# Kernel optimization log

Measured on AMD Instinct MI355X. Metric: run time of the kernel, lower is better.

The kernel has to match this reference:

```python
import jax, jax.numpy as jnp
import numpy as np
from jax import lax

KH = KW = 3
K = KH * KW
STRIDE = 1
PAD = 1
DIL = 1
GN_GROUPS = 32
EPS = 1e-5


def setup_inputs() -> dict:
    key = jax.random.key(0)
    k0, k1, k2 = jax.random.split(key, 3)
    B, C, H, W = 8, 256, 64, 64
    O = 256
    x = jax.random.normal(k0, (B, C, H, W), jnp.float32)
    # offset-predicting conv (DeformConv2dPack.conv_offset); small weights keep offsets ~O(1)
    w_off = jax.random.normal(k1, (2 * K, C, KH, KW), jnp.float32) * 0.01
    b_off = jnp.zeros((2 * K,), jnp.float32)
    w_dcn = jax.random.normal(k2, (O, C, KH, KW), jnp.float32) * (1.0 / np.sqrt(C * K))
    gamma = jnp.ones((O,), jnp.float32)
    beta = jnp.zeros((O,), jnp.float32)
    return {"x": x, "w_off": w_off, "b_off": b_off, "w_dcn": w_dcn, "gamma": gamma, "beta": beta}


def _deform_conv(x, w_off, b_off, w_dcn):
    B, C, H, W = x.shape
    O = w_dcn.shape[0]
    # offsets via standard conv: [B, 2K, Ho, Wo]; channel layout (k, (dy, dx))
    offset = lax.conv_general_dilated(
        x, w_off, (STRIDE, STRIDE), [(PAD, PAD), (PAD, PAD)],
        rhs_dilation=(DIL, DIL), dimension_numbers=("NCHW", "OIHW", "NCHW"))
    offset = offset + b_off[None, :, None, None]
    Ho, Wo = offset.shape[2], offset.shape[3]
    off = offset.reshape(B, K, 2, Ho, Wo)
    ky = jnp.repeat(jnp.arange(KH), KW)  # [K]
    kx = jnp.tile(jnp.arange(KW), KH)    # [K]
    base_y = (jnp.arange(Ho) * STRIDE - PAD)[None, :, None] + (ky * DIL)[:, None, None]  # [K,Ho,1]
    base_x = (jnp.arange(Wo) * STRIDE - PAD)[None, None, :] + (kx * DIL)[:, None, None]  # [K,1,Wo]
    py = off[:, :, 0] + base_y[None].astype(off.dtype)  # [B,K,Ho,Wo]
    px = off[:, :, 1] + base_x[None].astype(off.dtype)

    def sample_one(xi, py_i, px_i):  # xi [C,H,W]; py/px [K,Ho,Wo]
        y0 = jnp.floor(py_i)
        x0 = jnp.floor(px_i)
        dy = py_i - y0
        dx = px_i - x0
        y0i = y0.astype(jnp.int32)
        x0i = x0.astype(jnp.int32)

        def gather(yi, xj, w):
            valid = (yi >= 0) & (yi < H) & (xj >= 0) & (xj < W)
            yc = jnp.clip(yi, 0, H - 1)
            xc = jnp.clip(xj, 0, W - 1)
            return xi[:, yc, xc] * (w * valid)[None]  # [C,K,Ho,Wo]

        return (gather(y0i, x0i, (1 - dy) * (1 - dx))
                + gather(y0i, x0i + 1, (1 - dy) * dx)
                + gather(y0i + 1, x0i, dy * (1 - dx))
                + gather(y0i + 1, x0i + 1, dy * dx))

    cols = jax.vmap(sample_one)(x, py, px)  # [B,C,K,Ho,Wo]
    y = jnp.einsum("ock,bckp->bop", w_dcn.reshape(O, C, K),
                   cols.reshape(B, C, K, Ho * Wo))
    return y.reshape(B, O, Ho, Wo)


def _group_norm(y, gamma, beta):
    B, O, Ho, Wo = y.shape
    g = y.reshape(B, GN_GROUPS, O // GN_GROUPS, Ho, Wo)
    mean = g.mean(axis=(2, 3, 4), keepdims=True)
    var = g.var(axis=(2, 3, 4), keepdims=True)
    yn = ((g - mean) * lax.rsqrt(var + EPS)).reshape(B, O, Ho, Wo)
    return yn * gamma[None, :, None, None] + beta[None, :, None, None]


def reference(x, w_off, b_off, w_dcn, gamma, beta):
    y = _deform_conv(x, w_off, b_off, w_dcn)
    y = _group_norm(y, gamma, beta)
    return y * jnp.tanh(jax.nn.softplus(y))  # Mish
```

## Files before the change

### kernel.cpp

```cpp
#include <hip/hip_runtime.h>
#include <hip/hip_bf16.h>
#include <math.h>

typedef __bf16 bf16x8 __attribute__((ext_vector_type(8)));
typedef float f32x4 __attribute__((ext_vector_type(4)));
typedef unsigned int u32;
typedef u32 u32x4 __attribute__((ext_vector_type(4)));
typedef u32 u32x2 __attribute__((ext_vector_type(2)));


__device__ inline u32 pack2bf16(float a, float b) {
  u32 ua = __float_as_uint(a);
  u32 ub = __float_as_uint(b);
  ua += 0x7fffu + ((ua >> 16) & 1u);
  ub += 0x7fffu + ((ub >> 16) & 1u);
  return (ua >> 16) | (ub & 0xffff0000u);
}

__global__ void prep(const float* __restrict__ w_dcn, const float* __restrict__ w_off,
                     unsigned short* __restrict__ wT4, unsigned short* __restrict__ wOffT,
                     float* __restrict__ stats) {
  size_t id = (size_t)blockIdx.x * 256 + threadIdx.x;
  if (id < 589824) {
    int o  = (int)(id / 2304);
    int ck = (int)(id % 2304);
    int k = ck >> 8, c = ck & 255;
    float v = w_dcn[(size_t)(o * 256 + c) * 9 + k];
    u32 uv = __float_as_uint(v);
    uv += 0x7fffu + ((uv >> 16) & 1u);
    int tile = ck >> 6, kk = ck & 63;
    int lin = o * 128 + kk * 2;
    int swz = lin ^ ((o & 7) << 4);
    *(unsigned short*)((char*)wT4 + (size_t)tile * 32768 + swz) = (unsigned short)(uv >> 16);
  } else if (id < 663552) {
    int r = (int)(id - 589824);
    int tile = r >> 11;
    int rr = r & 2047;
    int o = rr >> 6, kk = rr & 63;
    int k = tile >> 2, cc = tile & 3;
    int c = (cc << 6) + kk;
    float v = (o < 18) ? w_off[(size_t)(o * 256 + c) * 9 + k] : 0.f;
    u32 uv = __float_as_uint(v);
    uv += 0x7fffu + ((uv >> 16) & 1u);
    int swz = (o * 128 + kk * 2) ^ ((o & 7) << 4);
    *(unsigned short*)((char*)wOffT + (size_t)tile * 4096 + swz) = (unsigned short)(uv >> 16);
  } else if (id < 664064) {
    stats[id - 663552] = 0.f;
  }
}

__global__ __launch_bounds__(256) void transpose_x(const float* __restrict__ x,
                                                   unsigned short* __restrict__ xT) {
  __shared__ float tl[64][65];
  int bx = blockIdx.x;
  int b = bx >> 8;
  int y = (bx >> 2) & 63;
  int cb = (bx & 3) << 6;
  int t = threadIdx.x;
  int xi = t & 63, cr = t >> 6;
  size_t base = (((size_t)(b * 256 + cb) * 64 + y) << 6);
#pragma unroll
  for (int rep = 0; rep < 16; ++rep) {
    int cl = rep * 4 + cr;
    tl[cl][xi] = x[base + (size_t)cl * 4096 + xi];
  }
  __syncthreads();
  int xw = t & 63, cpair = t >> 6;
#pragma unroll
  for (int r = 0; r < 2; ++r) {
    int cgl = cpair * 2 + r;
    int cg = (cb >> 3) + cgl;
    u32 pk4[4];
#pragma unroll
    for (int i = 0; i < 4; ++i)
      pk4[i] = pack2bf16(tl[cgl * 8 + 2 * i][xw], tl[cgl * 8 + 2 * i + 1][xw]);
    u32x4 v = {pk4[0], pk4[1], pk4[2], pk4[3]};
    *(u32x4*)((char*)xT + (((size_t)b << 21)) + ((size_t)cg << 16) + ((y << 6) + xw) * 16) = v;
  }
}

__global__ __launch_bounds__(512, 2) void conv_offset_mfma(
    const unsigned short* __restrict__ xT, const unsigned short* __restrict__ wOffT,
    float* __restrict__ offs) {
  __shared__ unsigned short A[2][128][64];
  __shared__ unsigned short Bo[2][2048];
  const int bx = blockIdx.x;
  const int lb = ((bx & 7) << 5) + (bx >> 3);
  const int b = lb >> 5;
  const int rp = lb & 31;
  const int t = threadIdx.x;
  const int lane = t & 63, wid = t >> 6;
  const char* xTbB = (const char*)xT + ((size_t)b << 21);
  const int p = t >> 2;
  const int row = (rp << 1) + (p >> 6);
  const int xx = p & 63;
  const int cpl = (t & 3) << 1;

  f32x4 acc[2];
  {
    f32x4 z = {0.f, 0.f, 0.f, 0.f};
    acc[0] = z; acc[1] = z;
  }

  u32x4 ra = {0u,0u,0u,0u}, rb = {0u,0u,0u,0u};

  auto issue = [&](int tt, int d) {
    int k = tt >> 2, cc = tt & 3;
    int ky = k / 3, kx = k - ky * 3;
    int ys = row - 1 + ky;
    int xs = xx - 1 + kx;
    bool ok = ((unsigned)ys < 64u) && ((unsigned)xs < 64u);
    u32x4 z = {0u,0u,0u,0u};
    ra = z; rb = z;
    if (ok) {
      const char* s0 = xTbB + ((size_t)(cc * 8 + cpl) << 16) + (((ys << 6) + xs) << 4);
      ra = *(const u32x4*)s0;
      rb = *(const u32x4*)(s0 + 65536);
    }
    if (wid < 4)
      __builtin_amdgcn_global_load_lds(
          (const __attribute__((address_space(1))) u32*)((const char*)wOffT + ((size_t)tt << 12) + (wid << 10) + (lane << 4)),
          (__attribute__((address_space(3))) u32*)((char*)&Bo[d][0] + (wid << 10)),
          16, 0, 0);
  };
  auto writeA = [&](int d) {
    char* dst = (char*)&A[d][0][0] + p * 128;
    int b0 = (t & 3) << 5;
    int sw = (p & 7) << 4;
    *(u32x4*)(dst + (b0 ^ sw)) = ra;
    *(u32x4*)(dst + ((b0 + 16) ^ sw)) = rb;
  };

  issue(0, 0);
  writeA(0);
  __syncthreads();

  int cur = 0;
  for (int tt = 0; tt < 36; ++tt) {
    if (tt < 35) issue(tt + 1, cur ^ 1);
#pragma unroll
    for (int s = 0; s < 2; ++s) {
      int r16 = (wid << 4) + (lane & 15);
      int kx = (s << 6) + ((lane >> 4) << 4);
      bf16x8 a = *(const bf16x8*)((const char*)&A[cur][0][0] + r16 * 128 + (kx ^ ((r16 & 7) << 4)));
#pragma unroll
      for (int j = 0; j < 2; ++j) {
        int o = (j << 4) + (lane & 15);
        bf16x8 bv = *(const bf16x8*)((const char*)&Bo[cur][0] + o * 128 + (kx ^ ((o & 7) << 4)));
        acc[j] = __builtin_amdgcn_mfma_f32_16x16x32_bf16(a, bv, acc[j], 0, 0, 0);
      }
    }
    if (tt < 35) writeA(cur ^ 1);
    __syncthreads();
    cur ^= 1;
  }

#pragma unroll
  for (int j = 0; j < 2; ++j) {
    int o = (j << 4) + (lane & 15);
    if (o < 18) {
#pragma unroll
      for (int r = 0; r < 4; ++r) {
        int pl = (wid << 4) + ((lane >> 4) << 2) + r;
        offs[((size_t)b * 4096 + (rp << 7) + pl) * 18 + o] = acc[j][r];
      }
    }
  }
}

union Arena {
  struct {
    unsigned short A[2][64][64];
    unsigned short Bt[2][16384];
  } m;
  unsigned short ytile[256][72];
};

__global__ __launch_bounds__(512, 4) void dcn_main(
    const unsigned short* __restrict__ xT, const float* __restrict__ offs,
    const float* __restrict__ boff, const unsigned short* __restrict__ wT4,
    unsigned short* __restrict__ yb, float* __restrict__ stats) {
  __shared__ Arena ar;

  const int bx = blockIdx.x;
  const int lb = ((bx & 7) << 6) + (bx >> 3);
  const int b = lb >> 6;
  const int row = lb & 63;
  const int pxbase = row << 6;
  const int t = threadIdx.x;
  const int lane = t & 63, wid = t >> 6;
  const char* xTbB = (const char*)xT + ((size_t)b << 21);
  const int ph = wid >> 2;
  const int obase = (wid & 3) << 6;

  f32x4 acc[2][4];
#pragma unroll
  for (int i = 0; i < 2; ++i)
#pragma unroll
    for (int j = 0; j < 4; ++j) {
      f32x4 z = {0.f, 0.f, 0.f, 0.f};
      acc[i][j] = z;
    }

  auto cparams = [&](int k, u32& c01, u32& c23, f32x4& w4) {
    int ky = k / 3, kx = k - ky * 3;
    const float* op = offs + ((size_t)b * 4096 + pxbase + lane) * 18 + k * 2;
    float py = op[0] + boff[k * 2] + (float)(row - 1 + ky);
    float pxf = op[1] + boff[k * 2 + 1] + (float)((lane & 63) - 1 + kx);
    float fy = floorf(py), fx = floorf(pxf);
    float dy = py - fy, dx = pxf - fx;
    int y0 = (int)fy, x0 = (int)fx;
    int y1 = y0 + 1, x1 = x0 + 1;
    float vy0 = ((unsigned)y0 < 64u) ? 1.f : 0.f;
    float vy1 = ((unsigned)y1 < 64u) ? 1.f : 0.f;
    float vx0 = ((unsigned)x0 < 64u) ? 1.f : 0.f;
    float vx1 = ((unsigned)x1 < 64u) ? 1.f : 0.f;
    int y0c = min(max(y0, 0), 63), y1c = min(max(y1, 0), 63);
    int x0c = min(max(x0, 0), 63), x1c = min(max(x1, 0), 63);
    c01 = (u32)((y0c << 6) + x0c) | ((u32)((y0c << 6) + x1c) << 16);
    c23 = (u32)((y1c << 6) + x0c) | ((u32)((y1c << 6) + x1c) << 16);
    w4[0] = (1.f - dy) * (1.f - dx) * vy0 * vx0;
    w4[1] = (1.f - dy) * dx * vy0 * vx1;
    w4[2] = dy * (1.f - dx) * vy1 * vx0;
    w4[3] = dy * dx * vy1 * vx1;
  };

  u32x4 r0, r1, r2, r3;

  auto issueAB = [&](int tt, int cc, int d, u32 c01, u32 c23) {
    {
      const char* src = (const char*)wT4 + ((size_t)tt << 15) + (wid << 12);
      char* dstb = (char*)&ar.m.Bt[d][0] + (wid << 12);
#pragma unroll
      for (int i2 = 0; i2 < 4; ++i2) {
        __builtin_amdgcn_global_load_lds(
            (const __attribute__((address_space(1))) u32*)(src + (i2 << 10) + (lane << 4)),
            (__attribute__((address_space(3))) u32*)(dstb + (i2 << 10)),
            16, 0, 0);
      }
    }
    const char* base = xTbB + ((size_t)((cc << 3) + wid) << 16);
    r0 = *(const u32x4*)(base + ((c01 & 0xffffu) << 4));
    r1 = *(const u32x4*)(base + ((c01 >> 16) << 4));
    r2 = *(const u32x4*)(base + ((c23 & 0xffffu) << 4));
    r3 = *(const u32x4*)(base + ((c23 >> 16) << 4));
  };
  auto packA = [&](int d, f32x4 w4) {
    float w0 = w4[0], w1 = w4[1], w2 = w4[2], w3 = w4[3];
    u32 o4[4];
#pragma unroll
    for (int e = 0; e < 4; ++e) {
      float lo = w0 * __uint_as_float(r0[e] << 16);
      lo = fmaf(w1, __uint_as_float(r1[e] << 16), lo);
      lo = fmaf(w2, __uint_as_float(r2[e] << 16), lo);
      lo = fmaf(w3, __uint_as_float(r3[e] << 16), lo);
      float hi = w0 * __uint_as_float(r0[e] & 0xffff0000u);
      hi = fmaf(w1, __uint_as_float(r1[e] & 0xffff0000u), hi);
      hi = fmaf(w2, __uint_as_float(r2[e] & 0xffff0000u), hi);
      hi = fmaf(w3, __uint_as_float(r3[e] & 0xffff0000u), hi);
      asm("v_cvt_pk_bf16_f32 %0, %1, %2" : "=v"(o4[e]) : "v"(lo), "v"(hi));
    }
    u32x4 ov = {o4[0], o4[1], o4[2], o4[3]};
    *(u32x4*)((char*)&ar.m.A[d][0][0] + lane * 128 + ((wid << 4) ^ ((lane & 7) << 4))) = ov;
  };

  u32 cur01, cur23, nxt01 = 0, nxt23 = 0;
  f32x4 curw, nxtw = {0.f, 0.f, 0.f, 0.f};
  cparams(0, cur01, cur23, curw);
  issueAB(0, 0, 0, cur01, cur23);
  packA(0, curw);
  __syncthreads();

  for (int k = 0; k < 9; ++k) {
    if (k < 8) cparams(k + 1, nxt01, nxt23, nxtw);
#pragma unroll
    for (int cc = 0; cc < 4; ++cc) {
      const int d = cc & 1;
      const int tt = (k << 2) + cc;
      const bool last = (tt == 35);
      f32x4 pkw = (cc < 3) ? curw : nxtw;
      if (!last)
        issueAB(tt + 1, (cc + 1) & 3, d ^ 1,
                (cc < 3) ? cur01 : nxt01, (cc < 3) ? cur23 : nxt23);
      {
        const char* Abase = (const char*)&ar.m.A[d][0][0];
        const char* Bbase = (const char*)&ar.m.Bt[d][0];
        __builtin_amdgcn_s_setprio(1);
#pragma unroll
        for (int s = 0; s < 2; ++s) {
          int kx = (s << 6) + ((lane >> 4) << 4);
          bf16x8 a[2], bb[4];
#pragma unroll
          for (int i = 0; i < 2; ++i) {
            int r16 = (ph << 5) + (i << 4) + (lane & 15);
            a[i] = *(const bf16x8*)(Abase + r16 * 128 + (kx ^ ((r16 & 7) << 4)));
          }
#pragma unroll
          for (int j = 0; j < 4; ++j) {
            int o = obase + (j << 4) + (lane & 15);
            bb[j] = *(const bf16x8*)(Bbase + o * 128 + (kx ^ ((o & 7) << 4)));
          }
#pragma unroll
          for (int i = 0; i < 2; ++i)
#pragma unroll
            for (int j = 0; j < 4; ++j)
              acc[i][j] = __builtin_amdgcn_mfma_f32_16x16x32_bf16(a[i], bb[j], acc[i][j], 0, 0, 0);
        }
        __builtin_amdgcn_s_setprio(0);
      }
      __builtin_amdgcn_sched_barrier(0);
      if (!last) packA(d ^ 1, pkw);
      __syncthreads();
    }
    cur01 = nxt01; cur23 = nxt23; curw = nxtw;
  }

#pragma unroll
  for (int j = 0; j < 4; ++j) {
    float s1 = 0.f, s2 = 0.f;
#pragma unroll
    for (int i = 0; i < 2; ++i)
#pragma unroll
      for (int r = 0; r < 4; ++r) {
        float v = acc[i][j][r];
        s1 += v;
        s2 += v * v;
      }
    s1 += __shfl_xor(s1, 1, 64);  s2 += __shfl_xor(s2, 1, 64);
    s1 += __shfl_xor(s1, 2, 64);  s2 += __shfl_xor(s2, 2, 64);
    s1 += __shfl_xor(s1, 4, 64);  s2 += __shfl_xor(s2, 4, 64);
    s1 += __shfl_xor(s1, 16, 64); s2 += __shfl_xor(s2, 16, 64);
    s1 += __shfl_xor(s1, 32, 64); s2 += __shfl_xor(s2, 32, 64);
    if ((lane & 0x37) == 0) {
      int g = (obase + (j << 4) + (lane & 15)) >> 3;
      atomicAdd(&stats[((b << 5) + g) * 2 + 0], s1);
      atomicAdd(&stats[((b << 5) + g) * 2 + 1], s2);
    }
  }

#pragma unroll
  for (int i = 0; i < 2; ++i)
#pragma unroll
    for (int j = 0; j < 4; ++j) {
      int o = obase + (j << 4) + (lane & 15);
      int pxr = (ph << 5) + (i << 4) + ((lane >> 4) << 2);
      u32 wv0, wv1;
      asm("v_cvt_pk_bf16_f32 %0, %1, %2" : "=v"(wv0) : "v"(acc[i][j][0]), "v"(acc[i][j][1]));
      asm("v_cvt_pk_bf16_f32 %0, %1, %2" : "=v"(wv1) : "v"(acc[i][j][2]), "v"(acc[i][j][3]));
      u32x2 wv = {wv0, wv1};
      *(u32x2*)((char*)ar.ytile + o * 144 + pxr * 2) = wv;
    }
  __syncthreads();
  {
    int o = t >> 1, half = t & 1;
    const char* srcb = (const char*)ar.ytile + o * 144 + (half << 6);
    unsigned short* dst = yb + (((size_t)(b * 256 + o)) << 12) + pxbase + (half << 5);
#pragma unroll
    for (int qq = 0; qq < 4; ++qq)
      *(u32x4*)((char*)dst + (qq << 4)) = *(const u32x4*)(srcb + (qq << 4));
  }
}

__global__ __launch_bounds__(256) void gn_mish(const unsigned short* __restrict__ yb,
                                               const float* __restrict__ stats,
                                               const float* __restrict__ gamma,
                                               const float* __restrict__ beta,
                                               float* __restrict__ out) {
  int v = blockIdx.x * 512 + threadIdx.x;
#pragma unroll
  for (int it = 0; it < 2; ++it, v += 256) {
    int o = (v >> 9) & 255;
    int b = v >> 17;
    float s1 = stats[((b << 5) + (o >> 3)) * 2 + 0];
    float s2 = stats[((b << 5) + (o >> 3)) * 2 + 1];
    float mean = s1 * (1.f / 32768.f);
    float var = s2 * (1.f / 32768.f) - mean * mean;
    float rstd = rsqrtf(var + 1e-5f);
    float ga = gamma[o] * rstd, be = beta[o] - mean * gamma[o] * rstd;
    u32x4 u = *(const u32x4*)(yb + ((size_t)v << 3));
    float res[8];
#pragma unroll
    for (int e = 0; e < 4; ++e) {
      float va = __uint_as_float(u[e] << 16);
      float vb = __uint_as_float(u[e] & 0xffff0000u);
      float v0 = fmaf(va, ga, be);
      float v1 = fmaf(vb, ga, be);
      float e0 = expf(fminf(v0, 15.f));
      float e1 = expf(fminf(v1, 15.f));
      float n0 = e0 * (e0 + 2.f);
      float n1 = e1 * (e1 + 2.f);
      float m0 = v0 * (n0 / (n0 + 2.f));
      float m1 = v1 * (n1 / (n1 + 2.f));
      if (v0 > 15.f) m0 = v0;
      if (v1 > 15.f) m1 = v1;
      res[2 * e] = m0;
      res[2 * e + 1] = m1;
    }
    f32x4 o0 = {res[0], res[1], res[2], res[3]};
    f32x4 o1 = {res[4], res[5], res[6], res[7]};
    float* dst = out + ((size_t)v << 3);
    *(f32x4*)dst = o0;
    *((f32x4*)dst + 1) = o1;
  }
}

extern "C" void kernel_launch(void* const* d_in, const int* in_sizes, int n_in,
                              void* d_out, int out_size, void* d_ws, size_t ws_size,
                              hipStream_t stream) {
  const float* x     = (const float*)d_in[0];
  const float* w_off = (const float*)d_in[1];
  const float* b_off = (const float*)d_in[2];
  const float* w_dcn = (const float*)d_in[3];
  const float* gamma = (const float*)d_in[4];
  const float* beta  = (const float*)d_in[5];
  float* out = (float*)d_out;
  char* ws = (char*)d_ws;
  unsigned short* xT   = (unsigned short*)(ws);
  unsigned short* yb   = (unsigned short*)(ws + 16777216);
  float* offs          = (float*)(ws + 33554432);
  unsigned short* wT4  = (unsigned short*)(ws + 35913728);
  unsigned short* wOffT= (unsigned short*)(ws + 37093376);
  float* stats         = (float*)(ws + 37240832);
  prep<<<dim3(2594), dim3(256), 0, stream>>>(w_dcn, w_off, wT4, wOffT, stats);
  transpose_x<<<dim3(2048), dim3(256), 0, stream>>>(x, xT);
  conv_offset_mfma<<<dim3(256), dim3(512), 0, stream>>>(xT, wOffT, offs);
  dcn_main<<<dim3(512), dim3(512), 0, stream>>>(xT, offs, b_off, wT4, yb, stats);
  gn_mish<<<dim3(2048), dim3(256), 0, stream>>>(yb, stats, gamma, beta, out);
}
```

Measured before the change: 139.6 us.

## Build deformable-sampled A operand in registers, drop LDS staging for A

The main DCN kernel now has each of 4 waves gather and bilinearly interpolate its own A fragments directly into MFMA operand registers, instead of writing a shared A tile to LDS and reading it back. The block shrinks from 512 to 256 threads, and each wave covers all 64 pixels against a 64-channel output slice. This removes the LDS round trip for A and the extra synchronisation around packA. The cost is that each wave repeats the gather work for its own output slice, about 4x redundant sampling, and register pressure rises with a 4x4 accumulator tile and 16 gathered vectors.

```diff
diff --git a/kernel.cpp b/kernel.cpp
--- a/kernel.cpp
+++ b/kernel.cpp
@@ -168,19 +168,16 @@
   }
 }
 
-union Arena {
-  struct {
-    unsigned short A[2][64][64];
-    unsigned short Bt[2][16384];
-  } m;
+union ArenaU {
+  unsigned short Bt[2][16384];
   unsigned short ytile[256][72];
 };
 
-__global__ __launch_bounds__(512, 4) void dcn_main(
+__global__ __launch_bounds__(256) void dcn_main(
     const unsigned short* __restrict__ xT, const float* __restrict__ offs,
     const float* __restrict__ boff, const unsigned short* __restrict__ wT4,
     unsigned short* __restrict__ yb, float* __restrict__ stats) {
-  __shared__ Arena ar;
+  __shared__ ArenaU ar;
 
   const int bx = blockIdx.x;
   const int lb = ((bx & 7) << 6) + (bx >> 3);
@@ -189,137 +186,123 @@
   const int pxbase = row << 6;
   const int t = threadIdx.x;
   const int lane = t & 63, wid = t >> 6;
+  const int obase = wid << 6;
+  const int pl = lane & 15;
+  const int gsub = lane >> 4;
   const char* xTbB = (const char*)xT + ((size_t)b << 21);
-  const int ph = wid >> 2;
-  const int obase = (wid & 3) << 6;
-
-  f32x4 acc[2][4];
-#pragma unroll
-  for (int i = 0; i < 2; ++i)
+
+  f32x4 acc[4][4];
+#pragma unroll
+  for (int i = 0; i < 4; ++i)
 #pragma unroll
     for (int j = 0; j < 4; ++j) {
       f32x4 z = {0.f, 0.f, 0.f, 0.f};
       acc[i][j] = z;
     }
 
-  auto cparams = [&](int k, u32& c01, u32& c23, f32x4& w4) {
+  u32 c01[4], c23[4];
+  f32x4 w4[4];
+  auto cparams = [&](int k) {
     int ky = k / 3, kx = k - ky * 3;
-    const float* op = offs + ((size_t)b * 4096 + pxbase + lane) * 18 + k * 2;
-    float py = op[0] + boff[k * 2] + (float)(row - 1 + ky);
-    float pxf = op[1] + boff[k * 2 + 1] + (float)((lane & 63) - 1 + kx);
-    float fy = floorf(py), fx = floorf(pxf);
-    float dy = py - fy, dx = pxf - fx;
-    int y0 = (int)fy, x0 = (int)fx;
-    int y1 = y0 + 1, x1 = x0 + 1;
-    float vy0 = ((unsigned)y0 < 64u) ? 1.f : 0.f;
-    float vy1 = ((unsigned)y1 < 64u) ? 1.f : 0.f;
-    float vx0 = ((unsigned)x0 < 64u) ? 1.f : 0.f;
-    float vx1 = ((unsigned)x1 < 64u) ? 1.f : 0.f;
-    int y0c = min(max(y0, 0), 63), y1c = min(max(y1, 0), 63);
-    int x0c = min(max(x0, 0), 63), x1c = min(max(x1, 0), 63);
-    c01 = (u32)((y0c << 6) + x0c) | ((u32)((y0c << 6) + x1c) << 16);
-    c23 = (u32)((y1c << 6) + x0c) | ((u32)((y1c << 6) + x1c) << 16);
-    w4[0] = (1.f - dy) * (1.f - dx) * vy0 * vx0;
-    w4[1] = (1.f - dy) * dx * vy0 * vx1;
-    w4[2] = dy * (1.f - dx) * vy1 * vx0;
-    w4[3] = dy * dx * vy1 * vx1;
+    float by = boff[k * 2], bxo = boff[k * 2 + 1];
+#pragma unroll
+    for (int i = 0; i < 4; ++i) {
+      int px = (i << 4) + pl;
+      const float* op = offs + ((size_t)b * 4096 + pxbase + px) * 18 + k * 2;
+      float py = op[0] + by + (float)(row - 1 + ky);
+      float pxf = op[1] + bxo + (float)(px - 1 + kx);
+      float fy = floorf(py), fx = floorf(pxf);
+      float dy = py - fy, dx = pxf - fx;
+      int y0 = (int)fy, x0 = (int)fx;
+      int y1 = y0 + 1, x1 = x0 + 1;
+      float vy0 = ((unsigned)y0 < 64u) ? 1.f : 0.f;
+      float vy1 = ((unsigned)y1 < 64u) ? 1.f : 0.f;
+      float vx0 = ((unsigned)x0 < 64u) ? 1.f : 0.f;
+      float vx1 = ((unsigned)x1 < 64u) ? 1.f : 0.f;
+      int y0c = min(max(y0, 0), 63), y1c = min(max(y1, 0), 63);
+      int x0c = min(max(x0, 0), 63), x1c = min(max(x1, 0), 63);
+      c01[i] = (u32)((y0c << 6) + x0c) | ((u32)((y0c << 6) + x1c) << 16);
+      c23[i] = (u32)((y1c << 6) + x0c) | ((u32)((y1c << 6) + x1c) << 16);
+      w4[i][0] = (1.f - dy) * (1.f - dx) * vy0 * vx0;
+      w4[i][1] = (1.f - dy) * dx * vy0 * vx1;
+      w4[i][2] = dy * (1.f - dx) * vy1 * vx0;
+      w4[i][3] = dy * dx * vy1 * vx1;
+    }
   };
 
-  u32x4 r0, r1, r2, r3;
-
-  auto issueAB = [&](int tt, int cc, int d, u32 c01, u32 c23) {
-    {
-      const char* src = (const char*)wT4 + ((size_t)tt << 15) + (wid << 12);
-      char* dstb = (char*)&ar.m.Bt[d][0] + (wid << 12);
-#pragma unroll
-      for (int i2 = 0; i2 < 4; ++i2) {
-        __builtin_amdgcn_global_load_lds(
-            (const __attribute__((address_space(1))) u32*)(src + (i2 << 10) + (lane << 4)),
-            (__attribute__((address_space(3))) u32*)(dstb + (i2 << 10)),
-            16, 0, 0);
+  auto stageB = [&](int tt, int d) {
+    const char* src = (const char*)wT4 + ((size_t)tt << 15) + (wid << 13);
+    char* dstb = (char*)&ar.Bt[d][0] + (wid << 13);
+#pragma unroll
+    for (int i2 = 0; i2 < 8; ++i2) {
+      __builtin_amdgcn_global_load_lds(
+          (const __attribute__((address_space(1))) u32*)(src + (i2 << 10) + (lane << 4)),
+          (__attribute__((address_space(3))) u32*)(dstb + (i2 << 10)),
+          16, 0, 0);
+    }
+  };
+
+  cparams(0);
+  stageB(0, 0);
+  __syncthreads();
+
+  for (int k = 0; k < 9; ++k) {
+    if (k) cparams(k);
+#pragma unroll
+    for (int cc = 0; cc < 4; ++cc) {
+      const int tt = (k << 2) + cc;
+      const int d = tt & 1;
+      if (tt < 35) stageB(tt + 1, d ^ 1);
+#pragma unroll
+      for (int s = 0; s < 2; ++s) {
+        const char* base = xTbB + ((size_t)((cc << 3) + (s << 2) + gsub) << 16);
+        u32x4 cr[4][4];
+#pragma unroll
+        for (int i = 0; i < 4; ++i) {
+          cr[i][0] = *(const u32x4*)(base + ((c01[i] & 0xffffu) << 4));
+          cr[i][1] = *(const u32x4*)(base + ((c01[i] >> 16) << 4));
+          cr[i][2] = *(const u32x4*)(base + ((c23[i] & 0xffffu) << 4));
+          cr[i][3] = *(const u32x4*)(base + ((c23[i] >> 16) << 4));
+        }
+        bf16x8 bb[4];
+        const int kx = (s << 6) + (gsub << 4);
+#pragma unroll
+        for (int j = 0; j < 4; ++j) {
+          int o = obase + (j << 4) + pl;
+          bb[j] = *(const bf16x8*)((const char*)&ar.Bt[d][0] + o * 128 + (kx ^ ((o & 7) << 4)));
+        }
+#pragma unroll
+        for (int i = 0; i < 4; ++i) {
+          float w0 = w4[i][0], w1 = w4[i][1], w2 = w4[i][2], w3 = w4[i][3];
+          u32 o4[4];
+#pragma unroll
+          for (int e = 0; e < 4; ++e) {
+            float lo = w0 * __uint_as_float(cr[i][0][e] << 16);
+            lo = fmaf(w1, __uint_as_float(cr[i][1][e] << 16), lo);
+            lo = fmaf(w2, __uint_as_float(cr[i][2][e] << 16), lo);
+            lo = fmaf(w3, __uint_as_float(cr[i][3][e] << 16), lo);
+            float hi = w0 * __uint_as_float(cr[i][0][e] & 0xffff0000u);
+            hi = fmaf(w1, __uint_as_float(cr[i][1][e] & 0xffff0000u), hi);
+            hi = fmaf(w2, __uint_as_float(cr[i][2][e] & 0xffff0000u), hi);
+            hi = fmaf(w3, __uint_as_float(cr[i][3][e] & 0xffff0000u), hi);
+            asm("v_cvt_pk_bf16_f32 %0, %1, %2" : "=v"(o4[e]) : "v"(lo), "v"(hi));
+          }
+          u32x4 av = {o4[0], o4[1], o4[2], o4[3]};
+          bf16x8 af = __builtin_bit_cast(bf16x8, av);
+#pragma unroll
+          for (int j = 0; j < 4; ++j)
+            acc[i][j] = __builtin_amdgcn_mfma_f32_16x16x32_bf16(af, bb[j], acc[i][j], 0, 0, 0);
+        }
       }
-    }
-    const char* base = xTbB + ((size_t)((cc << 3) + wid) << 16);
-    r0 = *(const u32x4*)(base + ((c01 & 0xffffu) << 4));
-    r1 = *(const u32x4*)(base + ((c01 >> 16) << 4));
-    r2 = *(const u32x4*)(base + ((c23 & 0xffffu) << 4));
-    r3 = *(const u32x4*)(base + ((c23 >> 16) << 4));
-  };
-  auto packA = [&](int d, f32x4 w4) {
-    float w0 = w4[0], w1 = w4[1], w2 = w4[2], w3 = w4[3];
-    u32 o4[4];
-#pragma unroll
-    for (int e = 0; e < 4; ++e) {
-      float lo = w0 * __uint_as_float(r0[e] << 16);
-      lo = fmaf(w1, __uint_as_float(r1[e] << 16), lo);
-      lo = fmaf(w2, __uint_as_float(r2[e] << 16), lo);
-      lo = fmaf(w3, __uint_as_float(r3[e] << 16), lo);
-      float hi = w0 * __uint_as_float(r0[e] & 0xffff0000u);
-      hi = fmaf(w1, __uint_as_float(r1[e] & 0xffff0000u), hi);
-      hi = fmaf(w2, __uint_as_float(r2[e] & 0xffff0000u), hi);
-      hi = fmaf(w3, __uint_as_float(r3[e] & 0xffff0000u), hi);
-      asm("v_cvt_pk_bf16_f32 %0, %1, %2" : "=v"(o4[e]) : "v"(lo), "v"(hi));
-    }
-    u32x4 ov = {o4[0], o4[1], o4[2], o4[3]};
-    *(u32x4*)((char*)&ar.m.A[d][0][0] + lane * 128 + ((wid << 4) ^ ((lane & 7) << 4))) = ov;
-  };
-
-  u32 cur01, cur23, nxt01 = 0, nxt23 = 0;
-  f32x4 curw, nxtw = {0.f, 0.f, 0.f, 0.f};
-  cparams(0, cur01, cur23, curw);
-  issueAB(0, 0, 0, cur01, cur23);
-  packA(0, curw);
-  __syncthreads();
-
-  for (int k = 0; k < 9; ++k) {
-    if (k < 8) cparams(k + 1, nxt01, nxt23, nxtw);
-#pragma unroll
-    for (int cc = 0; cc < 4; ++cc) {
-      const int d = cc & 1;
-      const int tt = (k << 2) + cc;
-      const bool last = (tt == 35);
-      f32x4 pkw = (cc < 3) ? curw : nxtw;
-      if (!last)
-        issueAB(tt + 1, (cc + 1) & 3, d ^ 1,
-                (cc < 3) ? cur01 : nxt01, (cc < 3) ? cur23 : nxt23);
-      {
-        const char* Abase = (const char*)&ar.m.A[d][0][0];
-        const char* Bbase = (const char*)&ar.m.Bt[d][0];
-        __builtin_amdgcn_s_setprio(1);
-#pragma unroll
-        for (int s = 0; s < 2; ++s) {
-          int kx = (s << 6) + ((lane >> 4) << 4);
-          bf16x8 a[2], bb[4];
-#pragma unroll
-          for (int i = 0; i < 2; ++i) {
-            int r16 = (ph << 5) + (i << 4) + (lane & 15);
-            a[i] = *(const bf16x8*)(Abase + r16 * 128 + (kx ^ ((r16 & 7) << 4)));
-          }
-#pragma unroll
-          for (int j = 0; j < 4; ++j) {
-            int o = obase + (j << 4) + (lane & 15);
-            bb[j] = *(const bf16x8*)(Bbase + o * 128 + (kx ^ ((o & 7) << 4)));
-          }
-#pragma unroll
-          for (int i = 0; i < 2; ++i)
-#pragma unroll
-            for (int j = 0; j < 4; ++j)
-              acc[i][j] = __builtin_amdgcn_mfma_f32_16x16x32_bf16(a[i], bb[j], acc[i][j], 0, 0, 0);
-        }
-        __builtin_amdgcn_s_setprio(0);
-      }
-      __builtin_amdgcn_sched_barrier(0);
-      if (!last) packA(d ^ 1, pkw);
       __syncthreads();
     }
-    cur01 = nxt01; cur23 = nxt23; curw = nxtw;
   }
 
 #pragma unroll
   for (int j = 0; j < 4; ++j) {
     float s1 = 0.f, s2 = 0.f;
 #pragma unroll
-    for (int i = 0; i < 2; ++i)
+    for (int i = 0; i < 4; ++i)
 #pragma unroll
       for (int r = 0; r < 4; ++r) {
         float v = acc[i][j][r];
@@ -339,11 +322,11 @@
   }
 
 #pragma unroll
-  for (int i = 0; i < 2; ++i)
+  for (int i = 0; i < 4; ++i)
 #pragma unroll
     for (int j = 0; j < 4; ++j) {
       int o = obase + (j << 4) + (lane & 15);
-      int pxr = (ph << 5) + (i << 4) + ((lane >> 4) << 2);
+      int pxr = (i << 4) + ((lane >> 4) << 2);
       u32 wv0, wv1;
       asm("v_cvt_pk_bf16_f32 %0, %1, %2" : "=v"(wv0) : "v"(acc[i][j][0]), "v"(acc[i][j][1]));
       asm("v_cvt_pk_bf16_f32 %0, %1, %2" : "=v"(wv1) : "v"(acc[i][j][2]), "v"(acc[i][j][3]));
@@ -352,11 +335,11 @@
     }
   __syncthreads();
   {
-    int o = t >> 1, half = t & 1;
-    const char* srcb = (const char*)ar.ytile + o * 144 + (half << 6);
-    unsigned short* dst = yb + (((size_t)(b * 256 + o)) << 12) + pxbase + (half << 5);
-#pragma unroll
-    for (int qq = 0; qq < 4; ++qq)
+    int o = t;
+    const char* srcb = (const char*)ar.ytile + o * 144;
+    unsigned short* dst = yb + (((size_t)(b * 256 + o)) << 12) + pxbase;
+#pragma unroll
+    for (int qq = 0; qq < 8; ++qq)
       *(u32x4*)((char*)dst + (qq << 4)) = *(const u32x4*)(srcb + (qq << 4));
   }
 }
@@ -424,6 +407,6 @@
   prep<<<dim3(2594), dim3(256), 0, stream>>>(w_dcn, w_off, wT4, wOffT, stats);
   transpose_x<<<dim3(2048), dim3(256), 0, stream>>>(x, xT);
   conv_offset_mfma<<<dim3(256), dim3(512), 0, stream>>>(xT, wOffT, offs);
-  dcn_main<<<dim3(512), dim3(512), 0, stream>>>(xT, offs, b_off, wT4, yb, stats);
+  dcn_main<<<dim3(512), dim3(256), 0, stream>>>(xT, offs, b_off, wT4, yb, stats);
   gn_mish<<<dim3(2048), dim3(256), 0, stream>>>(yb, stats, gamma, beta, out);
 }
```

New measurement: 249.8 us. +78.9%, slower.
